# Kernel optimization log

Measured on AMD Instinct MI355X. Metric: run time of the kernel, lower is better.

The kernel has to match this reference:

```python
import jax, jax.numpy as jnp
import numpy as np

N = 100000       # nodes
E = 3200000      # edges (avg degree 32)
IN = 64          # in_channels
HID = 32         # hidden_channels
HEADS = 2
OUT = 1
EPS = 1e-5       # LayerNorm eps
SLOPE = 0.2      # LeakyReLU negative slope (PyG default)


def setup_inputs() -> dict:
    key = jax.random.key(0)
    ks = jax.random.split(key, 18)
    def nrm(k, shape, scale=0.1):
        return jax.random.normal(k, shape, dtype=jnp.float32) * scale
    return {
        "x": jax.random.normal(ks[0], (N, IN), dtype=jnp.float32),
        "edge_index": jax.random.randint(ks[1], (2, E), 0, N, dtype=jnp.int64),
        # GATConv layer 1 (concat=True)
        "W1": nrm(ks[2], (IN, HEADS * HID)),
        "a_src1": nrm(ks[3], (HEADS, HID)),
        "a_dst1": nrm(ks[4], (HEADS, HID)),
        "b1": jnp.zeros((HEADS * HID,), jnp.float32),
        "ln1_g": jnp.ones((HEADS * HID,), jnp.float32),
        "ln1_b": jnp.zeros((HEADS * HID,), jnp.float32),
        # GATConv layer 2 (heads=1, concat=False)
        "W2": nrm(ks[5], (HEADS * HID, HID)),
        "a_src2": nrm(ks[6], (1, HID)),
        "a_dst2": nrm(ks[7], (1, HID)),
        "b2": jnp.zeros((HID,), jnp.float32),
        "ln2_g": jnp.ones((HID,), jnp.float32),
        "ln2_b": jnp.zeros((HID,), jnp.float32),
        # output Linear
        "Wout": nrm(ks[8], (HID, OUT)),
        "bout": jnp.zeros((OUT,), jnp.float32),
    }


def layer_norm(x, g, b):
    mu = jnp.mean(x, axis=-1, keepdims=True)
    var = jnp.mean(jnp.square(x - mu), axis=-1, keepdims=True)
    return (x - mu) * jax.lax.rsqrt(var + EPS) * g + b


def gat_conv(x, edge_index, W, a_src, a_dst, bias, heads, ch, concat):
    """PyG GATConv (add_self_loops=True, bias=True), eval mode (no dropout)."""
    n = x.shape[0]
    loop = jnp.arange(n, dtype=edge_index.dtype)
    src = jnp.concatenate([edge_index[0], loop])   # [E+N]
    dst = jnp.concatenate([edge_index[1], loop])   # [E+N]
    h = (x @ W).reshape(n, heads, ch)              # [N,H,C]
    al_src = jnp.sum(h * a_src, axis=-1)           # [N,H]
    al_dst = jnp.sum(h * a_dst, axis=-1)           # [N,H]
    logits = jax.nn.leaky_relu(al_src[src] + al_dst[dst], SLOPE)  # [E+N,H]
    # segment softmax over destination nodes
    m = jax.lax.stop_gradient(jax.ops.segment_max(logits, dst, num_segments=n))
    e = jnp.exp(logits - m[dst])
    denom = jax.ops.segment_sum(e, dst, num_segments=n)
    alpha = e / denom[dst]                         # [E+N,H]
    out = jax.ops.segment_sum(h[src] * alpha[:, :, None], dst, num_segments=n)  # [N,H,C]
    out = out.reshape(n, heads * ch) if concat else out.mean(axis=1)
    return out + bias


def reference(x, edge_index, W1, a_src1, a_dst1, b1, ln1_g, ln1_b,
              W2, a_src2, a_dst2, b2, ln2_g, ln2_b, Wout, bout):
    h = gat_conv(x, edge_index, W1, a_src1, a_dst1, b1, HEADS, HID, True)
    h = jax.nn.elu(layer_norm(h, ln1_g, ln1_b))
    h = gat_conv(h, edge_index, W2, a_src2, a_dst2, b2, 1, HID, False)
    h = jax.nn.elu(layer_norm(h, ln2_g, ln2_b))
    return h @ Wout + bout  # [N, OUT]
```

## Files before the change

kernel.cpp:

```cpp
#include <hip/hip_runtime.h>

#define EPS 1e-5f
#define SLOPE 0.2f
#define MAXK 512
#define SEGCAP 12288
#define PBATCH 8192

__device__ __forceinline__ float leaky(float z) {
    return fmaxf(z, 0.f) + SLOPE * fminf(z, 0.f);
}
__device__ __forceinline__ ushort f2bf(float f) {
    unsigned u = __float_as_uint(f);
    u += 0x7FFFu + ((u >> 16) & 1u);
    return (ushort)(u >> 16);
}
__device__ __forceinline__ float bf2f(ushort b) {
    return __uint_as_float(((unsigned)b) << 16);
}
__device__ __forceinline__ float blo(unsigned u) {
    return __uint_as_float(u << 16);
}
__device__ __forceinline__ float bhi(unsigned u) {
    return __uint_as_float(u & 0xffff0000u);
}

__global__ __launch_bounds__(1024) void fused1(
    const int* __restrict__ ei, int E, int K, int* __restrict__ segcnt,
    unsigned* __restrict__ part,
    const float* __restrict__ x, const float* __restrict__ W1,
    const float* __restrict__ as1, const float* __restrict__ ad1,
    ushort* __restrict__ h1b, float* __restrict__ al_s, float* __restrict__ al_d,
    int N, int EB) {
    __shared__ float smem[4096 + 64 * 68];
    int t = threadIdx.x;
    if ((int)blockIdx.x < EB) {
        int* h   = (int*)smem;
        int* gp  = h + 512;
        int* run = h + 1024;
        for (int i = t; i < K; i += 1024) { h[i] = 0; run[i] = 0; }
        __syncthreads();
        int base = blockIdx.x * PBATCH;
        int sv[PBATCH / 1024], dv[PBATCH / 1024];
#pragma unroll
        for (int j = 0; j < PBATCH / 1024; j++) {
            int e = base + j * 1024 + t;
            sv[j] = (e < E) ? ei[e] : -1;
            dv[j] = (e < E) ? ei[E + e] : -1;
            if (dv[j] >= 0) atomicAdd(&h[dv[j] >> 8], 1);
        }
        __syncthreads();
        for (int i = t; i < K; i += 1024)
            gp[i] = h[i] ? atomicAdd(&segcnt[i * 16], h[i]) : 0;
        __syncthreads();
#pragma unroll
        for (int j = 0; j < PBATCH / 1024; j++) {
            if (dv[j] >= 0) {
                int b = dv[j] >> 8;
                int p = atomicAdd(&run[b], 1) + gp[b];
                if (p < SEGCAP)
                    part[(size_t)b * SEGCAP + p] =
                        ((unsigned)sv[j] << 8) | (unsigned)(dv[j] & 255);
            }
        }
        return;
    }
    float* Ws = smem;
    float (*xs)[68] = (float(*)[68])(smem + 4096);
    for (int i = t; i < 4096; i += 1024) Ws[i] = W1[i];
    int base = (blockIdx.x - EB) * 64;
    {
        int rr = t >> 4, kk = t & 15;
        int gr = base + rr;
        float4 vx = (gr < N) ? ((const float4*)x)[(size_t)gr * 16 + kk]
                             : make_float4(0.f, 0.f, 0.f, 0.f);
        *(float4*)&xs[rr][kk * 4] = vx;
    }
    __syncthreads();
    int wv = t >> 6, c = t & 63;
    int r0 = base + wv * 4;
    float acc0 = 0.f, acc1 = 0.f, acc2 = 0.f, acc3 = 0.f;
#pragma unroll
    for (int k = 0; k < 64; k += 4) {
        float4 x0 = *(const float4*)&xs[wv * 4 + 0][k];
        float4 x1 = *(const float4*)&xs[wv * 4 + 1][k];
        float4 x2 = *(const float4*)&xs[wv * 4 + 2][k];
        float4 x3 = *(const float4*)&xs[wv * 4 + 3][k];
        float w0 = Ws[(k + 0) * 64 + c];
        float w1 = Ws[(k + 1) * 64 + c];
        float w2 = Ws[(k + 2) * 64 + c];
        float w3 = Ws[(k + 3) * 64 + c];
        acc0 = fmaf(x0.x, w0, acc0); acc1 = fmaf(x1.x, w0, acc1);
        acc2 = fmaf(x2.x, w0, acc2); acc3 = fmaf(x3.x, w0, acc3);
        acc0 = fmaf(x0.y, w1, acc0); acc1 = fmaf(x1.y, w1, acc1);
        acc2 = fmaf(x2.y, w1, acc2); acc3 = fmaf(x3.y, w1, acc3);
        acc0 = fmaf(x0.z, w2, acc0); acc1 = fmaf(x1.z, w2, acc1);
        acc2 = fmaf(x2.z, w2, acc2); acc3 = fmaf(x3.z, w2, acc3);
        acc0 = fmaf(x0.w, w3, acc0); acc1 = fmaf(x1.w, w3, acc1);
        acc2 = fmaf(x2.w, w3, acc2); acc3 = fmaf(x3.w, w3, acc3);
    }
    int head = c >> 5, cc = c & 31;
    float asc = as1[head * 32 + cc], adc = ad1[head * 32 + cc];
    float vs0 = acc0 * asc, vd0 = acc0 * adc;
    float vs1 = acc1 * asc, vd1 = acc1 * adc;
    float vs2 = acc2 * asc, vd2 = acc2 * adc;
    float vs3 = acc3 * asc, vd3 = acc3 * adc;
#pragma unroll
    for (int off = 1; off < 32; off <<= 1) {
        vs0 += __shfl_xor(vs0, off); vd0 += __shfl_xor(vd0, off);
        vs1 += __shfl_xor(vs1, off); vd1 += __shfl_xor(vd1, off);
        vs2 += __shfl_xor(vs2, off); vd2 += __shfl_xor(vd2, off);
        vs3 += __shfl_xor(vs3, off); vd3 += __shfl_xor(vd3, off);
    }
    if (r0 + 0 < N) h1b[(size_t)(r0 + 0) * 64 + c] = f2bf(acc0);
    if (r0 + 1 < N) h1b[(size_t)(r0 + 1) * 64 + c] = f2bf(acc1);
    if (r0 + 2 < N) h1b[(size_t)(r0 + 2) * 64 + c] = f2bf(acc2);
    if (r0 + 3 < N) h1b[(size_t)(r0 + 3) * 64 + c] = f2bf(acc3);
    if (cc == 0) {
        if (r0 + 0 < N) { al_s[(r0 + 0) * 2 + head] = vs0; al_d[(r0 + 0) * 2 + head] = vd0; }
        if (r0 + 1 < N) { al_s[(r0 + 1) * 2 + head] = vs1; al_d[(r0 + 1) * 2 + head] = vd1; }
        if (r0 + 2 < N) { al_s[(r0 + 2) * 2 + head] = vs2; al_d[(r0 + 2) * 2 + head] = vd2; }
        if (r0 + 3 < N) { al_s[(r0 + 3) * 2 + head] = vs3; al_d[(r0 + 3) * 2 + head] = vd3; }
    }
}

__global__ __launch_bounds__(1024) void sortseg(
    const int* __restrict__ segcnt, int N,
    unsigned* __restrict__ part, int* __restrict__ nodeofs, int* __restrict__ cnt,
    int* __restrict__ perm) {
    __shared__ int h2[4096];
    __shared__ int sc[256];
    __shared__ int ex[256];
    __shared__ unsigned outb[SEGCAP];
    int b = blockIdx.x, t = threadIdx.x;
    size_t base = (size_t)b * SEGCAP;
    int sz = min(segcnt[b * 16], SEGCAP);
    for (int i = t; i < 4096; i += 1024) h2[i] = 0;
    __syncthreads();
    for (int i = t; i < sz; i += 1024) {
        unsigned code = part[base + i];
        int key = ((code & 255) << 4) | ((code >> 21) & 15);
        atomicAdd(&h2[key], 1);
    }
    __syncthreads();
    int v = 0;
    if (t < 256) {
#pragma unroll
        for (int i = 0; i < 16; i++) v += h2[t * 16 + i];
        sc[t] = v;
    }
    __syncthreads();
    for (int off = 1; off < 256; off <<= 1) {
        int xv = (t < 256 && t >= off) ? sc[t - off] : 0;
        __syncthreads();
        if (t < 256) sc[t] += xv;
        __syncthreads();
    }
    if (t < 256) {
        int exv = sc[t] - v;
        int run = exv;
#pragma unroll
        for (int i = 0; i < 16; i++) {
            int lc = h2[t * 16 + i];
            h2[t * 16 + i] = run;
            run += lc;
        }
        int n = b * 256 + t;
        if (n < N) { cnt[n] = v; nodeofs[n] = (int)(base + exv); }
    }
    __syncthreads();
    for (int i = t; i < sz; i += 1024) {
        unsigned code = part[base + i];
        int key = ((code & 255) << 4) | ((code >> 21) & 15);
        int p = atomicAdd(&h2[key], 1);
        outb[p] = code >> 8;
    }
    __syncthreads();
    for (int i = t; i < sz; i += 1024) part[base + i] = outb[i];
    __syncthreads();
    if (t < 256) h2[t] = 0;
    __syncthreads();
    int n = b * 256 + t;
    int dbin = min(v, 255);
    if (t < 256 && n < N) atomicAdd(&h2[dbin], 1);
    __syncthreads();
    int hv = (t < 256) ? h2[t] : 0;
    if (t < 256) sc[t] = hv;
    __syncthreads();
    for (int off = 1; off < 256; off <<= 1) {
        int xv = (t < 256 && t >= off) ? sc[t - off] : 0;
        __syncthreads();
        if (t < 256) sc[t] += xv;
        __syncthreads();
    }
    if (t < 256) ex[t] = sc[t] - hv;
    __syncthreads();
    if (t < 256 && n < N) {
        int r = atomicAdd(&ex[dbin], 1);
        perm[b * 256 + r] = n;
    }
}

__global__ __launch_bounds__(256, 2) void aggB1(
    const ushort* __restrict__ h1b, const float* __restrict__ als,
    const float* __restrict__ ald, const int* __restrict__ nodeofs,
    const int* __restrict__ cnt, const unsigned* __restrict__ csr,
    const int* __restrict__ perm,
    const float* __restrict__ b1, const float* __restrict__ g1,
    const float* __restrict__ bb1, ushort* __restrict__ h1out, int N) {
    int lane = threadIdx.x & 63;
    int grp = lane >> 3, q = lane & 7;
    int gbase = grp << 3;
    int idx = blockIdx.x * 32 + (threadIdx.x >> 6) * 8 + grp;
    bool valid = idx < N;
    int nc = perm[min(idx, N - 1)];
    int head = q >> 2;
    const float2* als2 = (const float2*)als;
    const float2* ald2 = (const float2*)ald;
    float2 adv = ald2[nc], asv = als2[nc];
    float ad0 = adv.x, ad1v = adv.y;
    float wsf = __expf(leaky((head ? asv.y : asv.x) + (head ? ad1v : ad0)));
    const uint4* h4 = (const uint4*)h1b;
    uint4 hs = h4[(size_t)nc * 8 + q];
    float a0 = wsf * blo(hs.x), a1 = wsf * bhi(hs.x);
    float a2 = wsf * blo(hs.y), a3 = wsf * bhi(hs.y);
    float a4 = wsf * blo(hs.z), a5 = wsf * bhi(hs.z);
    float a6 = wsf * blo(hs.w), a7 = wsf * bhi(hs.w);
    float lp0 = 0.f, lp1 = 0.f;
    int ofs = valid ? nodeofs[nc] : 0;
    int deg = valid ? cnt[nc] : 0;
    int degm1 = max(deg - 1, 0);
    int degmax = deg;
    degmax = max(degmax, __shfl_xor(degmax, 8));
    degmax = max(degmax, __shfl_xor(degmax, 16));
    degmax = max(degmax, __shfl_xor(degmax, 32));
    int sq0 = 0, sq1 = 0;
    if (degmax > 0) {
        int j0 = ofs + min(q, degm1);
        int j1 = ofs + min(8 + q, degm1);
        sq0 = min((int)csr[j0], N - 1);
        sq1 = min((int)csr[j1], N - 1);
    }
    for (int eb = 0; eb < degmax; eb += 16) {
        int s0[8], s1[8];
#pragma unroll
        for (int jj = 0; jj < 8; jj++) {
            s0[jj] = __shfl(sq0, gbase + jj);
            s1[jj] = __shfl(sq1, gbase + jj);
        }
        float2 av0 = als2[sq0];
        float2 av1 = als2[sq1];
        int nsq0 = sq0, nsq1 = sq1;
        int ebn = eb + 16;
        if (ebn < degmax) {
            int j0 = ofs + min(ebn + q, degm1);
            int j1 = ofs + min(ebn + 8 + q, degm1);
            nsq0 = min((int)csr[j0], N - 1);
            nsq1 = min((int)csr[j1], N - 1);
        }
        uint4 r0[8], r1[8];
#pragma unroll
        for (int jj = 0; jj < 8; jj++) {
            r0[jj] = h4[(size_t)s0[jj] * 8 + q];
            r1[jj] = h4[(size_t)s1[jj] * 8 + q];
        }
        bool ev0 = (eb + q < deg), ev1 = (eb + 8 + q < deg);
        float w00 = ev0 ? __expf(leaky(av0.x + ad0)) : 0.f;
        float w10 = ev0 ? __expf(leaky(av0.y + ad1v)) : 0.f;
        float w01 = ev1 ? __expf(leaky(av1.x + ad0)) : 0.f;
        float w11 = ev1 ? __expf(leaky(av1.y + ad1v)) : 0.f;
        lp0 += w00 + w01;
        lp1 += w10 + w11;
        float wa[8], wb[8];
#pragma unroll
        for (int jj = 0; jj < 8; jj++) {
            float w00s = __shfl(w00, gbase + jj);
            float w10s = __shfl(w10, gbase + jj);
            float w01s = __shfl(w01, gbase + jj);
            float w11s = __shfl(w11, gbase + jj);
            wa[jj] = head ? w10s : w00s;
            wb[jj] = head ? w11s : w01s;
        }
#pragma unroll
        for (int jj = 0; jj < 8; jj++) {
            float w = wa[jj];
            uint4 h0 = r0[jj];
            a0 = fmaf(w, blo(h0.x), a0); a1 = fmaf(w, bhi(h0.x), a1);
            a2 = fmaf(w, blo(h0.y), a2); a3 = fmaf(w, bhi(h0.y), a3);
            a4 = fmaf(w, blo(h0.z), a4); a5 = fmaf(w, bhi(h0.z), a5);
            a6 = fmaf(w, blo(h0.w), a6); a7 = fmaf(w, bhi(h0.w), a7);
            float w2 = wb[jj];
            uint4 h1v = r1[jj];
            a0 = fmaf(w2, blo(h1v.x), a0); a1 = fmaf(w2, bhi(h1v.x), a1);
            a2 = fmaf(w2, blo(h1v.y), a2); a3 = fmaf(w2, bhi(h1v.y), a3);
            a4 = fmaf(w2, blo(h1v.z), a4); a5 = fmaf(w2, bhi(h1v.z), a5);
            a6 = fmaf(w2, blo(h1v.w), a6); a7 = fmaf(w2, bhi(h1v.w), a7);
        }
        sq0 = nsq0;
        sq1 = nsq1;
    }
#pragma unroll
    for (int off = 1; off < 8; off <<= 1) {
        lp0 += __shfl_xor(lp0, off);
        lp1 += __shfl_xor(lp1, off);
    }
    if (!valid) return;
    float l = (head ? lp1 : lp0) + wsf;
    float inv = 1.f / l;
    float4 bA = ((const float4*)b1)[2 * q];
    float4 bB = ((const float4*)b1)[2 * q + 1];
    float v0 = a0 * inv + bA.x, v1 = a1 * inv + bA.y;
    float v2 = a2 * inv + bA.z, v3 = a3 * inv + bA.w;
    float v4 = a4 * inv + bB.x, v5 = a5 * inv + bB.y;
    float v6 = a6 * inv + bB.z, v7 = a7 * inv + bB.w;
    float s1 = v0 + v1 + v2 + v3 + v4 + v5 + v6 + v7;
#pragma unroll
    for (int off = 1; off < 8; off <<= 1) s1 += __shfl_xor(s1, off);
    float mu = s1 * (1.f / 64.f);
    float d0 = v0 - mu, d1 = v1 - mu, d2 = v2 - mu, d3 = v3 - mu;
    float d4 = v4 - mu, d5 = v5 - mu, d6 = v6 - mu, d7 = v7 - mu;
    float s2v = d0 * d0 + d1 * d1 + d2 * d2 + d3 * d3
              + d4 * d4 + d5 * d5 + d6 * d6 + d7 * d7;
#pragma unroll
    for (int off = 1; off < 8; off <<= 1) s2v += __shfl_xor(s2v, off);
    float rs = rsqrtf(s2v * (1.f / 64.f) + EPS);
    float4 gA = ((const float4*)g1)[2 * q];
    float4 gB = ((const float4*)g1)[2 * q + 1];
    float4 cA = ((const float4*)bb1)[2 * q];
    float4 cB = ((const float4*)bb1)[2 * q + 1];
    float y0 = d0 * rs * gA.x + cA.x;
    float y1 = d1 * rs * gA.y + cA.y;
    float y2 = d2 * rs * gA.z + cA.z;
    float y3 = d3 * rs * gA.w + cA.w;
    float y4 = d4 * rs * gB.x + cB.x;
    float y5 = d5 * rs * gB.y + cB.y;
    float y6 = d6 * rs * gB.z + cB.z;
    float y7 = d7 * rs * gB.w + cB.w;
    y0 = (y0 > 0.f) ? y0 : (__expf(y0) - 1.f);
    y1 = (y1 > 0.f) ? y1 : (__expf(y1) - 1.f);
    y2 = (y2 > 0.f) ? y2 : (__expf(y2) - 1.f);
    y3 = (y3 > 0.f) ? y3 : (__expf(y3) - 1.f);
    y4 = (y4 > 0.f) ? y4 : (__expf(y4) - 1.f);
    y5 = (y5 > 0.f) ? y5 : (__expf(y5) - 1.f);
    y6 = (y6 > 0.f) ? y6 : (__expf(y6) - 1.f);
    y7 = (y7 > 0.f) ? y7 : (__expf(y7) - 1.f);
    uint4 ov;
    ov.x = (unsigned)f2bf(y0) | ((unsigned)f2bf(y1) << 16);
    ov.y = (unsigned)f2bf(y2) | ((unsigned)f2bf(y3) << 16);
    ov.z = (unsigned)f2bf(y4) | ((unsigned)f2bf(y5) << 16);
    ov.w = (unsigned)f2bf(y6) | ((unsigned)f2bf(y7) << 16);
    ((uint4*)h1out)[(size_t)nc * 8 + q] = ov;
}

__global__ __launch_bounds__(256) void prep2(
    const ushort* __restrict__ h1ob, const float* __restrict__ W2,
    const float* __restrict__ as2, const float* __restrict__ ad2,
    ushort* __restrict__ h2b, float* __restrict__ al_s, float* __restrict__ al_d, int N) {
    __shared__ float Ws[64 * 32];
    __shared__ float xs[32][68];
    int t = threadIdx.x;
    for (int i = t; i < 64 * 32; i += 256) Ws[i] = W2[i];
    int base = blockIdx.x * 32;
    const ushort4* hv4 = (const ushort4*)h1ob;
    for (int i = t; i < 512; i += 256) {
        int rr = i >> 4, kk = i & 15;
        int gr = base + rr;
        ushort4 u = (gr < N) ? hv4[(unsigned)gr * 16 + kk] : make_ushort4(0, 0, 0, 0);
        xs[rr][kk * 4 + 0] = bf2f(u.x);
        xs[rr][kk * 4 + 1] = bf2f(u.y);
        xs[rr][kk * 4 + 2] = bf2f(u.z);
        xs[rr][kk * 4 + 3] = bf2f(u.w);
    }
    __syncthreads();
    int wv = t >> 6;
    int lane = t & 63;
    int half = lane >> 5, c = lane & 31;
    int rbase = wv * 8 + half * 4;
    int r0 = base + rbase;
    float acc0 = 0.f, acc1 = 0.f, acc2 = 0.f, acc3 = 0.f;
#pragma unroll
    for (int k = 0; k < 64; k += 4) {
        float4 x0 = *(const float4*)&xs[rbase + 0][k];
        float4 x1 = *(const float4*)&xs[rbase + 1][k];
        float4 x2 = *(const float4*)&xs[rbase + 2][k];
        float4 x3 = *(const float4*)&xs[rbase + 3][k];
        float w0 = Ws[(k + 0) * 32 + c];
        float w1 = Ws[(k + 1) * 32 + c];
        float w2 = Ws[(k + 2) * 32 + c];
        float w3 = Ws[(k + 3) * 32 + c];
        acc0 = fmaf(x0.x, w0, acc0); acc1 = fmaf(x1.x, w0, acc1);
        acc2 = fmaf(x2.x, w0, acc2); acc3 = fmaf(x3.x, w0, acc3);
        acc0 = fmaf(x0.y, w1, acc0); acc1 = fmaf(x1.y, w1, acc1);
        acc2 = fmaf(x2.y, w1, acc2); acc3 = fmaf(x3.y, w1, acc3);
        acc0 = fmaf(x0.z, w2, acc0); acc1 = fmaf(x1.z, w2, acc1);
        acc2 = fmaf(x2.z, w2, acc2); acc3 = fmaf(x3.z, w2, acc3);
        acc0 = fmaf(x0.w, w3, acc0); acc1 = fmaf(x1.w, w3, acc1);
        acc2 = fmaf(x2.w, w3, acc2); acc3 = fmaf(x3.w, w3, acc3);
    }
    float asc = as2[c], adc = ad2[c];
    float vs0 = acc0 * asc, vd0 = acc0 * adc;
    float vs1 = acc1 * asc, vd1 = acc1 * adc;
    float vs2 = acc2 * asc, vd2 = acc2 * adc;
    float vs3 = acc3 * asc, vd3 = acc3 * adc;
#pragma unroll
    for (int off = 1; off < 32; off <<= 1) {
        vs0 += __shfl_xor(vs0, off); vd0 += __shfl_xor(vd0, off);
        vs1 += __shfl_xor(vs1, off); vd1 += __shfl_xor(vd1, off);
        vs2 += __shfl_xor(vs2, off); vd2 += __shfl_xor(vd2, off);
        vs3 += __shfl_xor(vs3, off); vd3 += __shfl_xor(vd3, off);
    }
    if (r0 + 0 < N) h2b[(size_t)(r0 + 0) * 32 + c] = f2bf(acc0);
    if (r0 + 1 < N) h2b[(size_t)(r0 + 1) * 32 + c] = f2bf(acc1);
    if (r0 + 2 < N) h2b[(size_t)(r0 + 2) * 32 + c] = f2bf(acc2);
    if (r0 + 3 < N) h2b[(size_t)(r0 + 3) * 32 + c] = f2bf(acc3);
    if (c == 0) {
        if (r0 + 0 < N) { al_s[r0 + 0] = vs0; al_d[r0 + 0] = vd0; }
        if (r0 + 1 < N) { al_s[r0 + 1] = vs1; al_d[r0 + 1] = vd1; }
        if (r0 + 2 < N) { al_s[r0 + 2] = vs2; al_d[r0 + 2] = vd2; }
        if (r0 + 3 < N) { al_s[r0 + 3] = vs3; al_d[r0 + 3] = vd3; }
    }
}

__global__ __launch_bounds__(256, 2) void aggB2(
    const ushort* __restrict__ h2b, const float* __restrict__ als,
    const float* __restrict__ ald, const int* __restrict__ nodeofs,
    const int* __restrict__ cnt, const unsigned* __restrict__ csr,
    const int* __restrict__ perm,
    const float* __restrict__ b2, const float* __restrict__ g2,
    const float* __restrict__ bb2, const float* __restrict__ Wout,
    const float* __restrict__ bout, float* __restrict__ out, int N) {
    int lane = threadIdx.x & 63;
    int grp = lane >> 3, q = lane & 7;
    int gbase = grp << 3;
    int idx = blockIdx.x * 32 + (threadIdx.x >> 6) * 8 + grp;
    bool valid = idx < N;
    int nc = perm[min(idx, N - 1)];
    float myad = ald[nc];
    float wsf = __expf(leaky(als[nc] + myad));
    const ushort4* h4 = (const ushort4*)h2b;
    ushort4 hs = h4[(unsigned)nc * 8 + q];
    float a0 = wsf * bf2f(hs.x), a1 = wsf * bf2f(hs.y);
    float a2 = wsf * bf2f(hs.z), a3 = wsf * bf2f(hs.w);
    float lp = 0.f;
    int ofs = valid ? nodeofs[nc] : 0;
    int deg = valid ? cnt[nc] : 0;
    int degm1 = max(deg - 1, 0);
    int degmax = deg;
    degmax = max(degmax, __shfl_xor(degmax, 8));
    degmax = max(degmax, __shfl_xor(degmax, 16));
    degmax = max(degmax, __shfl_xor(degmax, 32));
    int sq0 = 0, sq1 = 0;
    if (degmax > 0) {
        int j0 = ofs + min(q, degm1);
        int j1 = ofs + min(8 + q, degm1);
        sq0 = min((int)csr[j0], N - 1);
        sq1 = min((int)csr[j1], N - 1);
    }
    for (int eb = 0; eb < degmax; eb += 16) {
        int s0[8], s1[8];
#pragma unroll
        for (int jj = 0; jj < 8; jj++) {
            s0[jj] = __shfl(sq0, gbase + jj);
            s1[jj] = __shfl(sq1, gbase + jj);
        }
        float av0 = als[sq0];
        float av1 = als[sq1];
        int nsq0 = sq0, nsq1 = sq1;
        int ebn = eb + 16;
        if (ebn < degmax) {
            int j0 = ofs + min(ebn + q, degm1);
            int j1 = ofs + min(ebn + 8 + q, degm1);
            nsq0 = min((int)csr[j0], N - 1);
            nsq1 = min((int)csr[j1], N - 1);
        }
        ushort4 r0[8], r1[8];
#pragma unroll
        for (int jj = 0; jj < 8; jj++) {
            r0[jj] = h4[(unsigned)s0[jj] * 8 + q];
            r1[jj] = h4[(unsigned)s1[jj] * 8 + q];
        }
        float z0 = leaky(av0 + myad);
        float z1 = leaky(av1 + myad);
        float wq0 = (eb + q < deg) ? __expf(z0) : 0.f;
        float wq1 = (eb + 8 + q < deg) ? __expf(z1) : 0.f;
        lp += wq0 + wq1;
        float w0a[8], w1a[8];
#pragma unroll
        for (int jj = 0; jj < 8; jj++) {
            w0a[jj] = __shfl(wq0, gbase + jj);
            w1a[jj] = __shfl(wq1, gbase + jj);
        }
#pragma unroll
        for (int jj = 0; jj < 8; jj++) {
            float w0 = w0a[jj], w1 = w1a[jj];
            a0 = fmaf(w0, bf2f(r0[jj].x), a0);
            a1 = fmaf(w0, bf2f(r0[jj].y), a1);
            a2 = fmaf(w0, bf2f(r0[jj].z), a2);
            a3 = fmaf(w0, bf2f(r0[jj].w), a3);
            a0 = fmaf(w1, bf2f(r1[jj].x), a0);
            a1 = fmaf(w1, bf2f(r1[jj].y), a1);
            a2 = fmaf(w1, bf2f(r1[jj].z), a2);
            a3 = fmaf(w1, bf2f(r1[jj].w), a3);
        }
        sq0 = nsq0;
        sq1 = nsq1;
    }
#pragma unroll
    for (int off = 1; off < 8; off <<= 1) lp += __shfl_xor(lp, off);
    if (!valid) return;
    float l = lp + wsf;
    float inv = 1.f / l;
    float4 bv = ((const float4*)b2)[q];
    float v0 = a0 * inv + bv.x, v1 = a1 * inv + bv.y;
    float v2 = a2 * inv + bv.z, v3 = a3 * inv + bv.w;
    float s1 = v0 + v1 + v2 + v3;
#pragma unroll
    for (int off = 1; off < 8; off <<= 1) s1 += __shfl_xor(s1, off);
    float mu = s1 * (1.f / 32.f);
    float d0 = v0 - mu, d1 = v1 - mu, d2 = v2 - mu, d3 = v3 - mu;
    float s2v = d0 * d0 + d1 * d1 + d2 * d2 + d3 * d3;
#pragma unroll
    for (int off = 1; off < 8; off <<= 1) s2v += __shfl_xor(s2v, off);
    float rs = rsqrtf(s2v * (1.f / 32.f) + EPS);
    float4 gv = ((const float4*)g2)[q];
    float4 bbv = ((const float4*)bb2)[q];
    float y0 = d0 * rs * gv.x + bbv.x;
    float y1 = d1 * rs * gv.y + bbv.y;
    float y2 = d2 * rs * gv.z + bbv.z;
    float y3 = d3 * rs * gv.w + bbv.w;
    y0 = (y0 > 0.f) ? y0 : (__expf(y0) - 1.f);
    y1 = (y1 > 0.f) ? y1 : (__expf(y1) - 1.f);
    y2 = (y2 > 0.f) ? y2 : (__expf(y2) - 1.f);
    y3 = (y3 > 0.f) ? y3 : (__expf(y3) - 1.f);
    float4 wo = ((const float4*)Wout)[q];
    float p = y0 * wo.x + y1 * wo.y + y2 * wo.z + y3 * wo.w;
#pragma unroll
    for (int off = 1; off < 8; off <<= 1) p += __shfl_xor(p, off);
    if (q == 0) out[nc] = p + bout[0];
}

extern "C" void kernel_launch(void* const* d_in, const int* in_sizes, int n_in,
                              void* d_out, int out_size, void* d_ws, size_t ws_size,
                              hipStream_t stream) {
    const float* x    = (const float*)d_in[0];
    const int*   ei   = (const int*)d_in[1];
    const float* W1   = (const float*)d_in[2];
    const float* as1  = (const float*)d_in[3];
    const float* ad1  = (const float*)d_in[4];
    const float* b1   = (const float*)d_in[5];
    const float* g1   = (const float*)d_in[6];
    const float* bb1  = (const float*)d_in[7];
    const float* W2   = (const float*)d_in[8];
    const float* as2  = (const float*)d_in[9];
    const float* ad2  = (const float*)d_in[10];
    const float* b2   = (const float*)d_in[11];
    const float* g2   = (const float*)d_in[12];
    const float* bb2  = (const float*)d_in[13];
    const float* Wout = (const float*)d_in[14];
    const float* bout = (const float*)d_in[15];
    float* out = (float*)d_out;

    const int N = in_sizes[0] / 64;
    const int E = in_sizes[1] / 2;
    const int K = (N + 255) / 256;

    auto align_up = [](size_t v) { return (v + 255) & ~(size_t)255; };
    char* ws = (char*)d_ws;
    unsigned* part    = (unsigned*)ws; ws += align_up((size_t)K * SEGCAP * 4);
    int*      segcnt  = (int*)ws;      ws += align_up((size_t)MAXK * 16 * 4);
    int*      nodeofs = (int*)ws;      ws += align_up((size_t)N * 4);
    int*      cnt     = (int*)ws;      ws += align_up((size_t)N * 4);
    int*      perm    = (int*)ws;      ws += align_up((size_t)(K * 256) * 4);
    ushort*   h1b     = (ushort*)ws;   ws += align_up((size_t)N * 64 * 2);
    ushort*   h1ob    = (ushort*)ws;   ws += align_up((size_t)N * 64 * 2);
    ushort*   h2b     = (ushort*)ws;   ws += align_up((size_t)N * 32 * 2);
    float*    al1s    = (float*)ws;    ws += align_up((size_t)N * 2 * 4);
    float*    al1d    = (float*)ws;    ws += align_up((size_t)N * 2 * 4);
    float*    al2s    = (float*)ws;    ws += align_up((size_t)N * 4);
    float*    al2d    = (float*)ws;    ws += align_up((size_t)N * 4);

    const int EB = (E + PBATCH - 1) / PBATCH;
    const int PB = (N + 63) / 64;

    hipMemsetAsync(segcnt, 0, (size_t)K * 16 * 4, stream);
    fused1<<<EB + PB, 1024, 0, stream>>>(ei, E, K, segcnt, part,
                                         x, W1, as1, ad1, h1b, al1s, al1d, N, EB);
    sortseg<<<K, 1024, 0, stream>>>(segcnt, N, part, nodeofs, cnt, perm);
    aggB1<<<(N + 31) / 32, 256, 0, stream>>>(h1b, al1s, al1d, nodeofs, cnt, part,
                                             perm, b1, g1, bb1, h1ob, N);
    prep2<<<(N + 31) / 32, 256, 0, stream>>>(h1ob, W2, as2, ad2, h2b, al2s, al2d, N);
    aggB2<<<(N + 31) / 32, 256, 0, stream>>>(h2b, al2s, al2d, nodeofs, cnt, part,
                                             perm, b2, g2, bb2, Wout, bout, out, N);
}
```

Measured before the change: 314.8 us.

## Stage layer-1 neighbor feature gathers through LDS via global_load_lds

Replaces the register-held 16-edge gather in the layer-1 aggregation kernel with direct global-to-LDS 16-byte loads into a per-wave staging buffer of 8 slots, then reads the rows back from LDS for the weighted accumulation. The aim is to cut VGPR pressure from the large uint4 register arrays and raise occupancy; the launch-bounds minimum-blocks hint is dropped. In exchange each iteration handles 8 edges instead of 16, waits for all loads (vmcnt(0)) before computing, and adds LDS traffic plus a full memory drain per batch, which reduces how much load latency overlaps with compute.

```diff
diff --git a/kernel.cpp b/kernel.cpp
--- a/kernel.cpp
+++ b/kernel.cpp
@@ -5,6 +5,7 @@
 #define MAXK 512
 #define SEGCAP 12288
 #define PBATCH 8192
+#define AG1_SLOTS 8
 
 __device__ __forceinline__ float leaky(float z) {
     return fmaxf(z, 0.f) + SLOPE * fminf(z, 0.f);
@@ -22,6 +23,11 @@
 }
 __device__ __forceinline__ float bhi(unsigned u) {
     return __uint_as_float(u & 0xffff0000u);
+}
+__device__ __forceinline__ void gather16_to_lds(const void* g, void* l) {
+    __builtin_amdgcn_global_load_lds(
+        (const __attribute__((address_space(1))) void*)g,
+        (__attribute__((address_space(3))) void*)l, 16, 0, 0);
 }
 
 __global__ __launch_bounds__(1024) void fused1(
@@ -200,17 +206,20 @@
     }
 }
 
-__global__ __launch_bounds__(256, 2) void aggB1(
+__global__ __launch_bounds__(256) void aggB1(
     const ushort* __restrict__ h1b, const float* __restrict__ als,
     const float* __restrict__ ald, const int* __restrict__ nodeofs,
     const int* __restrict__ cnt, const unsigned* __restrict__ csr,
     const int* __restrict__ perm,
     const float* __restrict__ b1, const float* __restrict__ g1,
     const float* __restrict__ bb1, ushort* __restrict__ h1out, int N) {
-    int lane = threadIdx.x & 63;
+    __shared__ uint4 stage[4][AG1_SLOTS * 64];
+    int t = threadIdx.x;
+    int wid = t >> 6, lane = t & 63;
     int grp = lane >> 3, q = lane & 7;
     int gbase = grp << 3;
-    int idx = blockIdx.x * 32 + (threadIdx.x >> 6) * 8 + grp;
+    uint4* mystage = stage[wid];
+    int idx = blockIdx.x * 32 + wid * 8 + grp;
     bool valid = idx < N;
     int nc = perm[min(idx, N - 1)];
     int head = q >> 2;
@@ -233,70 +242,38 @@
     degmax = max(degmax, __shfl_xor(degmax, 8));
     degmax = max(degmax, __shfl_xor(degmax, 16));
     degmax = max(degmax, __shfl_xor(degmax, 32));
-    int sq0 = 0, sq1 = 0;
-    if (degmax > 0) {
-        int j0 = ofs + min(q, degm1);
-        int j1 = ofs + min(8 + q, degm1);
-        sq0 = min((int)csr[j0], N - 1);
-        sq1 = min((int)csr[j1], N - 1);
-    }
-    for (int eb = 0; eb < degmax; eb += 16) {
-        int s0[8], s1[8];
-#pragma unroll
-        for (int jj = 0; jj < 8; jj++) {
-            s0[jj] = __shfl(sq0, gbase + jj);
-            s1[jj] = __shfl(sq1, gbase + jj);
-        }
-        float2 av0 = als2[sq0];
-        float2 av1 = als2[sq1];
-        int nsq0 = sq0, nsq1 = sq1;
-        int ebn = eb + 16;
-        if (ebn < degmax) {
-            int j0 = ofs + min(ebn + q, degm1);
-            int j1 = ofs + min(ebn + 8 + q, degm1);
-            nsq0 = min((int)csr[j0], N - 1);
-            nsq1 = min((int)csr[j1], N - 1);
-        }
-        uint4 r0[8], r1[8];
-#pragma unroll
-        for (int jj = 0; jj < 8; jj++) {
-            r0[jj] = h4[(size_t)s0[jj] * 8 + q];
-            r1[jj] = h4[(size_t)s1[jj] * 8 + q];
-        }
-        bool ev0 = (eb + q < deg), ev1 = (eb + 8 + q < deg);
-        float w00 = ev0 ? __expf(leaky(av0.x + ad0)) : 0.f;
-        float w10 = ev0 ? __expf(leaky(av0.y + ad1v)) : 0.f;
-        float w01 = ev1 ? __expf(leaky(av1.x + ad0)) : 0.f;
-        float w11 = ev1 ? __expf(leaky(av1.y + ad1v)) : 0.f;
-        lp0 += w00 + w01;
-        lp1 += w10 + w11;
-        float wa[8], wb[8];
-#pragma unroll
-        for (int jj = 0; jj < 8; jj++) {
-            float w00s = __shfl(w00, gbase + jj);
-            float w10s = __shfl(w10, gbase + jj);
-            float w01s = __shfl(w01, gbase + jj);
-            float w11s = __shfl(w11, gbase + jj);
-            wa[jj] = head ? w10s : w00s;
-            wb[jj] = head ? w11s : w01s;
-        }
-#pragma unroll
-        for (int jj = 0; jj < 8; jj++) {
-            float w = wa[jj];
-            uint4 h0 = r0[jj];
-            a0 = fmaf(w, blo(h0.x), a0); a1 = fmaf(w, bhi(h0.x), a1);
-            a2 = fmaf(w, blo(h0.y), a2); a3 = fmaf(w, bhi(h0.y), a3);
-            a4 = fmaf(w, blo(h0.z), a4); a5 = fmaf(w, bhi(h0.z), a5);
-            a6 = fmaf(w, blo(h0.w), a6); a7 = fmaf(w, bhi(h0.w), a7);
-            float w2 = wb[jj];
-            uint4 h1v = r1[jj];
-            a0 = fmaf(w2, blo(h1v.x), a0); a1 = fmaf(w2, bhi(h1v.x), a1);
-            a2 = fmaf(w2, blo(h1v.y), a2); a3 = fmaf(w2, bhi(h1v.y), a3);
-            a4 = fmaf(w2, blo(h1v.z), a4); a5 = fmaf(w2, bhi(h1v.z), a5);
-            a6 = fmaf(w2, blo(h1v.w), a6); a7 = fmaf(w2, bhi(h1v.w), a7);
-        }
-        sq0 = nsq0;
-        sq1 = nsq1;
+    int sq = 0;
+    if (degmax > 0) sq = min((int)csr[ofs + min(q, degm1)], N - 1);
+    for (int eb = 0; eb < degmax; eb += AG1_SLOTS) {
+#pragma unroll
+        for (int k = 0; k < AG1_SLOTS; k++) {
+            int s = __shfl(sq, gbase + k);
+            gather16_to_lds(h4 + ((size_t)s * 8 + q), &mystage[k * 64]);
+        }
+        float2 av = als2[sq];
+        int nsq = sq;
+        int ebn = eb + AG1_SLOTS;
+        if (ebn < degmax)
+            nsq = min((int)csr[ofs + min(ebn + q, degm1)], N - 1);
+        bool ev = (eb + q < deg);
+        float w0 = ev ? __expf(leaky(av.x + ad0)) : 0.f;
+        float w1 = ev ? __expf(leaky(av.y + ad1v)) : 0.f;
+        lp0 += w0;
+        lp1 += w1;
+        asm volatile("s_waitcnt vmcnt(0)" ::: "memory");
+        __builtin_amdgcn_sched_barrier(0);
+#pragma unroll
+        for (int k = 0; k < AG1_SLOTS; k++) {
+            float wk0 = __shfl(w0, gbase + k);
+            float wk1 = __shfl(w1, gbase + k);
+            float w = head ? wk1 : wk0;
+            uint4 hv = mystage[k * 64 + lane];
+            a0 = fmaf(w, blo(hv.x), a0); a1 = fmaf(w, bhi(hv.x), a1);
+            a2 = fmaf(w, blo(hv.y), a2); a3 = fmaf(w, bhi(hv.y), a3);
+            a4 = fmaf(w, blo(hv.z), a4); a5 = fmaf(w, bhi(hv.z), a5);
+            a6 = fmaf(w, blo(hv.w), a6); a7 = fmaf(w, bhi(hv.w), a7);
+        }
+        sq = nsq;
     }
 #pragma unroll
     for (int off = 1; off < 8; off <<= 1) {
```

New measurement: 312.2 us. No clear change (-0.8%).

## Split layer-1 features per head and aggregate each head in separate blocks

Applied to the files above, without the earlier changes.

Stores the layer-1 projected features and attention scores in a head-major layout, so each head's features form a contiguous 64-byte row. The aggregation kernel now runs one head per block, with interleaved block indices pairing heads over the same node tiles. Each gather fetches half the bytes, aiming for better cache locality and less register pressure. In exchange, edge index and score loads are duplicated across heads. LayerNorm and ELU move into prep2, which adds an fp32 intermediate buffer round trip.

```diff
diff --git a/kernel.cpp b/kernel.cpp
--- a/kernel.cpp
+++ b/kernel.cpp
@@ -111,15 +111,17 @@
         vs2 += __shfl_xor(vs2, off); vd2 += __shfl_xor(vd2, off);
         vs3 += __shfl_xor(vs3, off); vd3 += __shfl_xor(vd3, off);
     }
-    if (r0 + 0 < N) h1b[(size_t)(r0 + 0) * 64 + c] = f2bf(acc0);
-    if (r0 + 1 < N) h1b[(size_t)(r0 + 1) * 64 + c] = f2bf(acc1);
-    if (r0 + 2 < N) h1b[(size_t)(r0 + 2) * 64 + c] = f2bf(acc2);
-    if (r0 + 3 < N) h1b[(size_t)(r0 + 3) * 64 + c] = f2bf(acc3);
+    size_t hb = (size_t)head * N * 32;
+    if (r0 + 0 < N) h1b[hb + (size_t)(r0 + 0) * 32 + cc] = f2bf(acc0);
+    if (r0 + 1 < N) h1b[hb + (size_t)(r0 + 1) * 32 + cc] = f2bf(acc1);
+    if (r0 + 2 < N) h1b[hb + (size_t)(r0 + 2) * 32 + cc] = f2bf(acc2);
+    if (r0 + 3 < N) h1b[hb + (size_t)(r0 + 3) * 32 + cc] = f2bf(acc3);
     if (cc == 0) {
-        if (r0 + 0 < N) { al_s[(r0 + 0) * 2 + head] = vs0; al_d[(r0 + 0) * 2 + head] = vd0; }
-        if (r0 + 1 < N) { al_s[(r0 + 1) * 2 + head] = vs1; al_d[(r0 + 1) * 2 + head] = vd1; }
-        if (r0 + 2 < N) { al_s[(r0 + 2) * 2 + head] = vs2; al_d[(r0 + 2) * 2 + head] = vd2; }
-        if (r0 + 3 < N) { al_s[(r0 + 3) * 2 + head] = vs3; al_d[(r0 + 3) * 2 + head] = vd3; }
+        size_t ab = (size_t)head * N;
+        if (r0 + 0 < N) { al_s[ab + r0 + 0] = vs0; al_d[ab + r0 + 0] = vd0; }
+        if (r0 + 1 < N) { al_s[ab + r0 + 1] = vs1; al_d[ab + r0 + 1] = vd1; }
+        if (r0 + 2 < N) { al_s[ab + r0 + 2] = vs2; al_d[ab + r0 + 2] = vd2; }
+        if (r0 + 3 < N) { al_s[ab + r0 + 3] = vs3; al_d[ab + r0 + 3] = vd3; }
     }
 }
 
@@ -200,32 +202,29 @@
     }
 }
 
-__global__ __launch_bounds__(256, 2) void aggB1(
+__global__ __launch_bounds__(256) void aggB1(
     const ushort* __restrict__ h1b, const float* __restrict__ als,
     const float* __restrict__ ald, const int* __restrict__ nodeofs,
     const int* __restrict__ cnt, const unsigned* __restrict__ csr,
-    const int* __restrict__ perm,
-    const float* __restrict__ b1, const float* __restrict__ g1,
-    const float* __restrict__ bb1, ushort* __restrict__ h1out, int N) {
+    const int* __restrict__ perm, const float* __restrict__ b1,
+    float* __restrict__ h1agg, int N) {
+    int bid = blockIdx.x;
+    int head = (bid >> 2) & 1;
+    int nblk = (bid >> 3) * 4 + (bid & 3);
     int lane = threadIdx.x & 63;
     int grp = lane >> 3, q = lane & 7;
     int gbase = grp << 3;
-    int idx = blockIdx.x * 32 + (threadIdx.x >> 6) * 8 + grp;
+    int idx = nblk * 32 + (threadIdx.x >> 6) * 8 + grp;
     bool valid = idx < N;
     int nc = perm[min(idx, N - 1)];
-    int head = q >> 2;
-    const float2* als2 = (const float2*)als;
-    const float2* ald2 = (const float2*)ald;
-    float2 adv = ald2[nc], asv = als2[nc];
-    float ad0 = adv.x, ad1v = adv.y;
-    float wsf = __expf(leaky((head ? asv.y : asv.x) + (head ? ad1v : ad0)));
-    const uint4* h4 = (const uint4*)h1b;
-    uint4 hs = h4[(size_t)nc * 8 + q];
-    float a0 = wsf * blo(hs.x), a1 = wsf * bhi(hs.x);
-    float a2 = wsf * blo(hs.y), a3 = wsf * bhi(hs.y);
-    float a4 = wsf * blo(hs.z), a5 = wsf * bhi(hs.z);
-    float a6 = wsf * blo(hs.w), a7 = wsf * bhi(hs.w);
-    float lp0 = 0.f, lp1 = 0.f;
+    const float* alsH = als + (size_t)head * N;
+    float adh = (ald + (size_t)head * N)[nc];
+    float wsf = __expf(leaky(alsH[nc] + adh));
+    const ushort4* hT = (const ushort4*)(h1b + (size_t)head * N * 32);
+    ushort4 hs = hT[(size_t)nc * 8 + q];
+    float a0 = wsf * bf2f(hs.x), a1 = wsf * bf2f(hs.y);
+    float a2 = wsf * bf2f(hs.z), a3 = wsf * bf2f(hs.w);
+    float lp = 0.f;
     int ofs = valid ? nodeofs[nc] : 0;
     int deg = valid ? cnt[nc] : 0;
     int degm1 = max(deg - 1, 0);
@@ -235,10 +234,8 @@
     degmax = max(degmax, __shfl_xor(degmax, 32));
     int sq0 = 0, sq1 = 0;
     if (degmax > 0) {
-        int j0 = ofs + min(q, degm1);
-        int j1 = ofs + min(8 + q, degm1);
-        sq0 = min((int)csr[j0], N - 1);
-        sq1 = min((int)csr[j1], N - 1);
+        sq0 = min((int)csr[ofs + min(q, degm1)], N - 1);
+        sq1 = min((int)csr[ofs + min(8 + q, degm1)], N - 1);
     }
     for (int eb = 0; eb < degmax; eb += 16) {
         int s0[8], s1[8];
@@ -247,112 +244,60 @@
             s0[jj] = __shfl(sq0, gbase + jj);
             s1[jj] = __shfl(sq1, gbase + jj);
         }
-        float2 av0 = als2[sq0];
-        float2 av1 = als2[sq1];
+        float av0 = alsH[sq0];
+        float av1 = alsH[sq1];
         int nsq0 = sq0, nsq1 = sq1;
         int ebn = eb + 16;
         if (ebn < degmax) {
-            int j0 = ofs + min(ebn + q, degm1);
-            int j1 = ofs + min(ebn + 8 + q, degm1);
-            nsq0 = min((int)csr[j0], N - 1);
-            nsq1 = min((int)csr[j1], N - 1);
-        }
-        uint4 r0[8], r1[8];
-#pragma unroll
-        for (int jj = 0; jj < 8; jj++) {
-            r0[jj] = h4[(size_t)s0[jj] * 8 + q];
-            r1[jj] = h4[(size_t)s1[jj] * 8 + q];
-        }
-        bool ev0 = (eb + q < deg), ev1 = (eb + 8 + q < deg);
-        float w00 = ev0 ? __expf(leaky(av0.x + ad0)) : 0.f;
-        float w10 = ev0 ? __expf(leaky(av0.y + ad1v)) : 0.f;
-        float w01 = ev1 ? __expf(leaky(av1.x + ad0)) : 0.f;
-        float w11 = ev1 ? __expf(leaky(av1.y + ad1v)) : 0.f;
-        lp0 += w00 + w01;
-        lp1 += w10 + w11;
-        float wa[8], wb[8];
-#pragma unroll
-        for (int jj = 0; jj < 8; jj++) {
-            float w00s = __shfl(w00, gbase + jj);
-            float w10s = __shfl(w10, gbase + jj);
-            float w01s = __shfl(w01, gbase + jj);
-            float w11s = __shfl(w11, gbase + jj);
-            wa[jj] = head ? w10s : w00s;
-            wb[jj] = head ? w11s : w01s;
-        }
-#pragma unroll
-        for (int jj = 0; jj < 8; jj++) {
-            float w = wa[jj];
-            uint4 h0 = r0[jj];
-            a0 = fmaf(w, blo(h0.x), a0); a1 = fmaf(w, bhi(h0.x), a1);
-            a2 = fmaf(w, blo(h0.y), a2); a3 = fmaf(w, bhi(h0.y), a3);
-            a4 = fmaf(w, blo(h0.z), a4); a5 = fmaf(w, bhi(h0.z), a5);
-            a6 = fmaf(w, blo(h0.w), a6); a7 = fmaf(w, bhi(h0.w), a7);
-            float w2 = wb[jj];
-            uint4 h1v = r1[jj];
-            a0 = fmaf(w2, blo(h1v.x), a0); a1 = fmaf(w2, bhi(h1v.x), a1);
-            a2 = fmaf(w2, blo(h1v.y), a2); a3 = fmaf(w2, bhi(h1v.y), a3);
-            a4 = fmaf(w2, blo(h1v.z), a4); a5 = fmaf(w2, bhi(h1v.z), a5);
-            a6 = fmaf(w2, blo(h1v.w), a6); a7 = fmaf(w2, bhi(h1v.w), a7);
+            nsq0 = min((int)csr[ofs + min(ebn + q, degm1)], N - 1);
+            nsq1 = min((int)csr[ofs + min(ebn + 8 + q, degm1)], N - 1);
+        }
+        ushort4 r0[8], r1[8];
+#pragma unroll
+        for (int jj = 0; jj < 8; jj++) {
+            r0[jj] = hT[(size_t)s0[jj] * 8 + q];
+            r1[jj] = hT[(size_t)s1[jj] * 8 + q];
+        }
+        float wq0 = (eb + q < deg) ? __expf(leaky(av0 + adh)) : 0.f;
+        float wq1 = (eb + 8 + q < deg) ? __expf(leaky(av1 + adh)) : 0.f;
+        lp += wq0 + wq1;
+        float w0a[8], w1a[8];
+#pragma unroll
+        for (int jj = 0; jj < 8; jj++) {
+            w0a[jj] = __shfl(wq0, gbase + jj);
+            w1a[jj] = __shfl(wq1, gbase + jj);
+        }
+#pragma unroll
+        for (int jj = 0; jj < 8; jj++) {
+            float w0 = w0a[jj], w1 = w1a[jj];
+            a0 = fmaf(w0, bf2f(r0[jj].x), a0);
+            a1 = fmaf(w0, bf2f(r0[jj].y), a1);
+            a2 = fmaf(w0, bf2f(r0[jj].z), a2);
+            a3 = fmaf(w0, bf2f(r0[jj].w), a3);
+            a0 = fmaf(w1, bf2f(r1[jj].x), a0);
+            a1 = fmaf(w1, bf2f(r1[jj].y), a1);
+            a2 = fmaf(w1, bf2f(r1[jj].z), a2);
+            a3 = fmaf(w1, bf2f(r1[jj].w), a3);
         }
         sq0 = nsq0;
         sq1 = nsq1;
     }
 #pragma unroll
-    for (int off = 1; off < 8; off <<= 1) {
-        lp0 += __shfl_xor(lp0, off);
-        lp1 += __shfl_xor(lp1, off);
-    }
+    for (int off = 1; off < 8; off <<= 1) lp += __shfl_xor(lp, off);
     if (!valid) return;
-    float l = (head ? lp1 : lp0) + wsf;
-    float inv = 1.f / l;
-    float4 bA = ((const float4*)b1)[2 * q];
-    float4 bB = ((const float4*)b1)[2 * q + 1];
-    float v0 = a0 * inv + bA.x, v1 = a1 * inv + bA.y;
-    float v2 = a2 * inv + bA.z, v3 = a3 * inv + bA.w;
-    float v4 = a4 * inv + bB.x, v5 = a5 * inv + bB.y;
-    float v6 = a6 * inv + bB.z, v7 = a7 * inv + bB.w;
-    float s1 = v0 + v1 + v2 + v3 + v4 + v5 + v6 + v7;
-#pragma unroll
-    for (int off = 1; off < 8; off <<= 1) s1 += __shfl_xor(s1, off);
-    float mu = s1 * (1.f / 64.f);
-    float d0 = v0 - mu, d1 = v1 - mu, d2 = v2 - mu, d3 = v3 - mu;
-    float d4 = v4 - mu, d5 = v5 - mu, d6 = v6 - mu, d7 = v7 - mu;
-    float s2v = d0 * d0 + d1 * d1 + d2 * d2 + d3 * d3
-              + d4 * d4 + d5 * d5 + d6 * d6 + d7 * d7;
-#pragma unroll
-    for (int off = 1; off < 8; off <<= 1) s2v += __shfl_xor(s2v, off);
-    float rs = rsqrtf(s2v * (1.f / 64.f) + EPS);
-    float4 gA = ((const float4*)g1)[2 * q];
-    float4 gB = ((const float4*)g1)[2 * q + 1];
-    float4 cA = ((const float4*)bb1)[2 * q];
-    float4 cB = ((const float4*)bb1)[2 * q + 1];
-    float y0 = d0 * rs * gA.x + cA.x;
-    float y1 = d1 * rs * gA.y + cA.y;
-    float y2 = d2 * rs * gA.z + cA.z;
-    float y3 = d3 * rs * gA.w + cA.w;
-    float y4 = d4 * rs * gB.x + cB.x;
-    float y5 = d5 * rs * gB.y + cB.y;
-    float y6 = d6 * rs * gB.z + cB.z;
-    float y7 = d7 * rs * gB.w + cB.w;
-    y0 = (y0 > 0.f) ? y0 : (__expf(y0) - 1.f);
-    y1 = (y1 > 0.f) ? y1 : (__expf(y1) - 1.f);
-    y2 = (y2 > 0.f) ? y2 : (__expf(y2) - 1.f);
-    y3 = (y3 > 0.f) ? y3 : (__expf(y3) - 1.f);
-    y4 = (y4 > 0.f) ? y4 : (__expf(y4) - 1.f);
-    y5 = (y5 > 0.f) ? y5 : (__expf(y5) - 1.f);
-    y6 = (y6 > 0.f) ? y6 : (__expf(y6) - 1.f);
-    y7 = (y7 > 0.f) ? y7 : (__expf(y7) - 1.f);
-    uint4 ov;
-    ov.x = (unsigned)f2bf(y0) | ((unsigned)f2bf(y1) << 16);
-    ov.y = (unsigned)f2bf(y2) | ((unsigned)f2bf(y3) << 16);
-    ov.z = (unsigned)f2bf(y4) | ((unsigned)f2bf(y5) << 16);
-    ov.w = (unsigned)f2bf(y6) | ((unsigned)f2bf(y7) << 16);
-    ((uint4*)h1out)[(size_t)nc * 8 + q] = ov;
+    float inv = 1.f / (lp + wsf);
+    float4 bv = ((const float4*)b1)[head * 8 + q];
+    float4 o;
+    o.x = a0 * inv + bv.x;
+    o.y = a1 * inv + bv.y;
+    o.z = a2 * inv + bv.z;
+    o.w = a3 * inv + bv.w;
+    ((float4*)h1agg)[(size_t)nc * 16 + head * 8 + q] = o;
 }
 
 __global__ __launch_bounds__(256) void prep2(
-    const ushort* __restrict__ h1ob, const float* __restrict__ W2,
+    const float* __restrict__ h1agg, const float* __restrict__ g1,
+    const float* __restrict__ bb1, const float* __restrict__ W2,
     const float* __restrict__ as2, const float* __restrict__ ad2,
     ushort* __restrict__ h2b, float* __restrict__ al_s, float* __restrict__ al_d, int N) {
     __shared__ float Ws[64 * 32];
@@ -360,15 +305,46 @@
     int t = threadIdx.x;
     for (int i = t; i < 64 * 32; i += 256) Ws[i] = W2[i];
     int base = blockIdx.x * 32;
-    const ushort4* hv4 = (const ushort4*)h1ob;
-    for (int i = t; i < 512; i += 256) {
-        int rr = i >> 4, kk = i & 15;
-        int gr = base + rr;
-        ushort4 u = (gr < N) ? hv4[(unsigned)gr * 16 + kk] : make_ushort4(0, 0, 0, 0);
-        xs[rr][kk * 4 + 0] = bf2f(u.x);
-        xs[rr][kk * 4 + 1] = bf2f(u.y);
-        xs[rr][kk * 4 + 2] = bf2f(u.z);
-        xs[rr][kk * 4 + 3] = bf2f(u.w);
+    {
+        int r = t >> 3, q = t & 7;
+        int gr = base + r;
+        const float4* h4 = (const float4*)h1agg;
+        float4 uA = make_float4(0.f, 0.f, 0.f, 0.f), uB = uA;
+        if (gr < N) {
+            uA = h4[(size_t)gr * 16 + q * 2 + 0];
+            uB = h4[(size_t)gr * 16 + q * 2 + 1];
+        }
+        float s = uA.x + uA.y + uA.z + uA.w + uB.x + uB.y + uB.z + uB.w;
+        s += __shfl_xor(s, 1); s += __shfl_xor(s, 2); s += __shfl_xor(s, 4);
+        float mu = s * (1.f / 64.f);
+        float d0 = uA.x - mu, d1 = uA.y - mu, d2 = uA.z - mu, d3 = uA.w - mu;
+        float d4 = uB.x - mu, d5 = uB.y - mu, d6 = uB.z - mu, d7 = uB.w - mu;
+        float s2 = d0 * d0 + d1 * d1 + d2 * d2 + d3 * d3
+                 + d4 * d4 + d5 * d5 + d6 * d6 + d7 * d7;
+        s2 += __shfl_xor(s2, 1); s2 += __shfl_xor(s2, 2); s2 += __shfl_xor(s2, 4);
+        float rs = rsqrtf(s2 * (1.f / 64.f) + EPS);
+        float4 gA = ((const float4*)g1)[q * 2 + 0];
+        float4 gB = ((const float4*)g1)[q * 2 + 1];
+        float4 cA = ((const float4*)bb1)[q * 2 + 0];
+        float4 cB = ((const float4*)bb1)[q * 2 + 1];
+        float y0 = d0 * rs * gA.x + cA.x;
+        float y1 = d1 * rs * gA.y + cA.y;
+        float y2 = d2 * rs * gA.z + cA.z;
+        float y3 = d3 * rs * gA.w + cA.w;
+        float y4 = d4 * rs * gB.x + cB.x;
+        float y5 = d5 * rs * gB.y + cB.y;
+        float y6 = d6 * rs * gB.z + cB.z;
+        float y7 = d7 * rs * gB.w + cB.w;
+        y0 = (y0 > 0.f) ? y0 : (__expf(y0) - 1.f);
+        y1 = (y1 > 0.f) ? y1 : (__expf(y1) - 1.f);
+        y2 = (y2 > 0.f) ? y2 : (__expf(y2) - 1.f);
+        y3 = (y3 > 0.f) ? y3 : (__expf(y3) - 1.f);
+        y4 = (y4 > 0.f) ? y4 : (__expf(y4) - 1.f);
+        y5 = (y5 > 0.f) ? y5 : (__expf(y5) - 1.f);
+        y6 = (y6 > 0.f) ? y6 : (__expf(y6) - 1.f);
+        y7 = (y7 > 0.f) ? y7 : (__expf(y7) - 1.f);
+        *(float4*)&xs[r][q * 8 + 0] = make_float4(y0, y1, y2, y3);
+        *(float4*)&xs[r][q * 8 + 4] = make_float4(y4, y5, y6, y7);
     }
     __syncthreads();
     int wv = t >> 6;
@@ -571,7 +547,7 @@
     int*      cnt     = (int*)ws;      ws += align_up((size_t)N * 4);
     int*      perm    = (int*)ws;      ws += align_up((size_t)(K * 256) * 4);
     ushort*   h1b     = (ushort*)ws;   ws += align_up((size_t)N * 64 * 2);
-    ushort*   h1ob    = (ushort*)ws;   ws += align_up((size_t)N * 64 * 2);
+    float*    h1agg   = (float*)ws;    ws += align_up((size_t)N * 64 * 4);
     ushort*   h2b     = (ushort*)ws;   ws += align_up((size_t)N * 32 * 2);
     float*    al1s    = (float*)ws;    ws += align_up((size_t)N * 2 * 4);
     float*    al1d    = (float*)ws;    ws += align_up((size_t)N * 2 * 4);
@@ -580,14 +556,17 @@
 
     const int EB = (E + PBATCH - 1) / PBATCH;
     const int PB = (N + 63) / 64;
+    const int NB1 = (N + 31) / 32;
+    const int G1 = ((NB1 + 3) / 4) * 8;
 
     hipMemsetAsync(segcnt, 0, (size_t)K * 16 * 4, stream);
     fused1<<<EB + PB, 1024, 0, stream>>>(ei, E, K, segcnt, part,
                                          x, W1, as1, ad1, h1b, al1s, al1d, N, EB);
     sortseg<<<K, 1024, 0, stream>>>(segcnt, N, part, nodeofs, cnt, perm);
-    aggB1<<<(N + 31) / 32, 256, 0, stream>>>(h1b, al1s, al1d, nodeofs, cnt, part,
-                                             perm, b1, g1, bb1, h1ob, N);
-    prep2<<<(N + 31) / 32, 256, 0, stream>>>(h1ob, W2, as2, ad2, h2b, al2s, al2d, N);
+    aggB1<<<G1, 256, 0, stream>>>(h1b, al1s, al1d, nodeofs, cnt, part,
+                                  perm, b1, h1agg, N);
+    prep2<<<(N + 31) / 32, 256, 0, stream>>>(h1agg, g1, bb1, W2, as2, ad2,
+                                             h2b, al2s, al2d, N);
     aggB2<<<(N + 31) / 32, 256, 0, stream>>>(h2b, al2s, al2d, nodeofs, cnt, part,
                                              perm, b2, g2, bb2, Wout, bout, out, N);
 }
```

After: 343.0 us. 1.09x slower.
